# Optimization experiments

Measured on AMD Instinct MI355X. Metric: run time of the kernel, lower is better.

Reference implementation:

```python
import jax, jax.numpy as jnp
import numpy as np

VOXEL_SIZE = (0.2, 0.2, 0.2)
PC_RANGE = (-51.2, -51.2, -3.0, 51.2, 51.2, 3.0)


def setup_inputs() -> dict:
    key = jax.random.key(0)
    # scale so a realistic fraction of points fall outside the z-range / xy-range
    points = jax.random.normal(key, (8, 1_000_000, 3), dtype=jnp.float32) * 20.0
    return {"points": points}


def reference(points):
    # points: [B, N, 3] (x, y, z)
    vs = jnp.asarray(VOXEL_SIZE, dtype=points.dtype)            # [3]
    pcr = jnp.asarray(PC_RANGE, dtype=points.dtype)             # [6]
    min_pt = pcr[:3]
    grid = jnp.round((pcr[3:] - pcr[:3]) / vs).astype(jnp.int32)  # [3] = (512,512,30)

    B, N, _ = points.shape

    # NaN filter (torch: drop rows with any NaN; here: mask them out)
    not_nan = ~jnp.isnan(points).any(axis=-1)                   # [B, N]
    p = jnp.where(not_nan[..., None], points, 0.0)              # NaN-safe points

    # dynamic voxelization: per-point integer voxel coord in (x, y, z) order
    coords_xyz = jnp.floor((p - min_pt) / vs).astype(jnp.int32)  # [B, N, 3]
    in_range = jnp.all((coords_xyz >= 0) & (coords_xyz < grid), axis=-1)  # [B, N]

    valid = not_nan & in_range                                   # [B, N]

    # voxelizer output convention is (z, y, x); invalid points get -1 (as in mmcv)
    coords_zyx = jnp.where(valid[..., None], coords_xyz[..., ::-1], -1)  # [B, N, 3] int32

    # point offsets from voxel centers (computed in x,y,z order, matching
    # torch's voxel_coords[:, [2,1,0]] un-permute)
    centers = coords_xyz.astype(points.dtype) * vs + min_pt + vs / 2
    point_offsets = jnp.where(valid[..., None], p - centers, 0.0)  # [B, N, 3]

    out_points = jnp.where(valid[..., None], p, 0.0)               # [B, N, 3]
    point_idxes = jnp.where(valid, jnp.arange(N, dtype=jnp.int32)[None, :], -1)  # [B, N]

    # masked (fixed-shape) analogue of the per-batch compacted dicts:
    # (points, voxel_coords, point_idxes, point_offsets, valid_mask)
    return out_points, coords_zyx, point_idxes, point_offsets, valid
```

## Files before the change

kernel.cpp:

```cpp
#include <hip/hip_runtime.h>
#include <stdint.h>


#define NPB   1000000
#define TOT   8000000
#define BLK   256
#define PPT   2
#define PPB   (BLK * PPT)
#define NBLK  (TOT / PPB)
#define F4PR  (PPB * 3 / 4)

typedef float fx4 __attribute__((ext_vector_type(4)));

__global__ __launch_bounds__(256, 8) void voxelize_kernel(
        const float* __restrict__ pts, float* __restrict__ out) {
    __shared__ __attribute__((aligned(16))) float lsA[PPB * 3];
    __shared__ __attribute__((aligned(16))) float lsB[PPB * 3];
    __shared__ __attribute__((aligned(16))) float lsC[PPB * 3];

    const int t = threadIdx.x;
    const uint32_t P0 = (uint32_t)blockIdx.x * PPB;

    const double R = 1.0 / (double)0.2f;

    const uint32_t n0  = P0 + (uint32_t)t;
    const uint32_t b0  = n0 / NPB;
    const uint32_t ni0 = n0 - b0 * NPB;

#pragma unroll
    for (int j = 0; j < PPT; ++j) {
        int      pb = j * BLK + t;
        uint32_t n  = P0 + pb;
        uint32_t ni = ni0 + (uint32_t)(j * BLK);
        if (ni >= NPB) ni -= NPB;

        const float* pp = pts + (size_t)n * 3;
        float x = pp[0], y = pp[1], z = pp[2];

        bool nn = (x == x) && (y == y) && (z == z);
        float px = nn ? x : 0.0f;
        float py = nn ? y : 0.0f;
        float pz = nn ? z : 0.0f;

        float tx = (float)((double)(px + 51.2f) * R);
        float ty = (float)((double)(py + 51.2f) * R);
        float tz = (float)((double)(pz + 3.0f)  * R);

        bool valid = nn && (tx >= 0.0f) && (tx < 512.0f)
                        && (ty >= 0.0f) && (ty < 512.0f)
                        && (tz >= 0.0f) && (tz < 30.0f);

        float fcx = truncf(tx);
        float fcy = truncf(ty);
        float fcz = truncf(tz);

        float ctx = (fcx * 0.2f + (-51.2f)) + 0.1f;
        float cty = (fcy * 0.2f + (-51.2f)) + 0.1f;
        float ctz = (fcz * 0.2f + (-3.0f))  + 0.1f;

        lsA[3*pb+0] = valid ? px : 0.0f;
        lsA[3*pb+1] = valid ? py : 0.0f;
        lsA[3*pb+2] = valid ? pz : 0.0f;
        lsB[3*pb+0] = valid ? fcz : -1.0f;
        lsB[3*pb+1] = valid ? fcy : -1.0f;
        lsB[3*pb+2] = valid ? fcx : -1.0f;
        lsC[3*pb+0] = valid ? (px - ctx) : 0.0f;
        lsC[3*pb+1] = valid ? (py - cty) : 0.0f;
        lsC[3*pb+2] = valid ? (pz - ctz) : 0.0f;

        out[(size_t)48000000 + n] = valid ? (float)ni : -1.0f;
        out[(size_t)80000000 + n] = valid ? 1.0f : 0.0f;
    }

    __syncthreads();

    size_t f40 = (size_t)blockIdx.x * F4PR;
#pragma unroll
    for (int i = 0; i < 2; ++i) {
        int li = i * BLK + t;
        if (li < F4PR) {
            size_t f4i = f40 + li;
            fx4 a = ((const fx4*)lsA)[li];
            fx4 c = ((const fx4*)lsB)[li];
            fx4 o = ((const fx4*)lsC)[li];
            ((fx4*)(out))[f4i]                    = a;
            ((fx4*)(out + (size_t)24000000))[f4i] = c;
            ((fx4*)(out + (size_t)56000000))[f4i] = o;
        }
    }
}

extern "C" void kernel_launch(void* const* d_in, const int* in_sizes, int n_in,
                              void* d_out, int out_size, void* d_ws, size_t ws_size,
                              hipStream_t stream) {
    const float* pts = (const float*)d_in[0];
    float* out = (float*)d_out;
    voxelize_kernel<<<NBLK, BLK, 0, stream>>>(pts, out);
}
```

Before: 406.4 us.

## Replace block-wide LDS transpose with per-wavefront staging and wave barriers

Each wavefront now stages its own 64 points' outputs in a private LDS slice and writes them out as float4 vectors right after computing them. This replaces the block-wide __syncthreads and second store loop with wave-level barriers. It also cuts LDS use per block, which may allow more resident blocks, and overlaps stores with computation across iterations. The risk is that wave_barrier ordering of LDS traffic within a wavefront is relied on, and only 48 of 64 lanes store in the vector phase.

```diff
diff --git a/kernel.cpp b/kernel.cpp
--- a/kernel.cpp
+++ b/kernel.cpp
@@ -8,17 +8,19 @@
 #define PPT   2
 #define PPB   (BLK * PPT)
 #define NBLK  (TOT / PPB)
-#define F4PR  (PPB * 3 / 4)
+#define NW    (BLK / 64)
 
 typedef float fx4 __attribute__((ext_vector_type(4)));
 
 __global__ __launch_bounds__(256, 8) void voxelize_kernel(
         const float* __restrict__ pts, float* __restrict__ out) {
-    __shared__ __attribute__((aligned(16))) float lsA[PPB * 3];
-    __shared__ __attribute__((aligned(16))) float lsB[PPB * 3];
-    __shared__ __attribute__((aligned(16))) float lsC[PPB * 3];
+    __shared__ __attribute__((aligned(16))) float lsA[NW * 192];
+    __shared__ __attribute__((aligned(16))) float lsB[NW * 192];
+    __shared__ __attribute__((aligned(16))) float lsC[NW * 192];
 
     const int t = threadIdx.x;
+    const int w = t >> 6;
+    const int l = t & 63;
     const uint32_t P0 = (uint32_t)blockIdx.x * PPB;
 
     const double R = 1.0 / (double)0.2f;
@@ -27,10 +29,13 @@
     const uint32_t b0  = n0 / NPB;
     const uint32_t ni0 = n0 - b0 * NPB;
 
+    float* lA = lsA + w * 192;
+    float* lB = lsB + w * 192;
+    float* lC = lsC + w * 192;
+
 #pragma unroll
     for (int j = 0; j < PPT; ++j) {
-        int      pb = j * BLK + t;
-        uint32_t n  = P0 + pb;
+        uint32_t n  = P0 + (uint32_t)(j * BLK) + (uint32_t)t;
         uint32_t ni = ni0 + (uint32_t)(j * BLK);
         if (ni >= NPB) ni -= NPB;
 
@@ -58,35 +63,33 @@
         float cty = (fcy * 0.2f + (-51.2f)) + 0.1f;
         float ctz = (fcz * 0.2f + (-3.0f))  + 0.1f;
 
-        lsA[3*pb+0] = valid ? px : 0.0f;
-        lsA[3*pb+1] = valid ? py : 0.0f;
-        lsA[3*pb+2] = valid ? pz : 0.0f;
-        lsB[3*pb+0] = valid ? fcz : -1.0f;
-        lsB[3*pb+1] = valid ? fcy : -1.0f;
-        lsB[3*pb+2] = valid ? fcx : -1.0f;
-        lsC[3*pb+0] = valid ? (px - ctx) : 0.0f;
-        lsC[3*pb+1] = valid ? (py - cty) : 0.0f;
-        lsC[3*pb+2] = valid ? (pz - ctz) : 0.0f;
+        lA[3*l+0] = valid ? px : 0.0f;
+        lA[3*l+1] = valid ? py : 0.0f;
+        lA[3*l+2] = valid ? pz : 0.0f;
+        lB[3*l+0] = valid ? fcz : -1.0f;
+        lB[3*l+1] = valid ? fcy : -1.0f;
+        lB[3*l+2] = valid ? fcx : -1.0f;
+        lC[3*l+0] = valid ? (px - ctx) : 0.0f;
+        lC[3*l+1] = valid ? (py - cty) : 0.0f;
+        lC[3*l+2] = valid ? (pz - ctz) : 0.0f;
 
-        out[(size_t)48000000 + n] = valid ? (float)ni : -1.0f;
-        out[(size_t)80000000 + n] = valid ? 1.0f : 0.0f;
-    }
+        __builtin_amdgcn_wave_barrier();
 
-    __syncthreads();
-
-    size_t f40 = (size_t)blockIdx.x * F4PR;
-#pragma unroll
-    for (int i = 0; i < 2; ++i) {
-        int li = i * BLK + t;
-        if (li < F4PR) {
-            size_t f4i = f40 + li;
-            fx4 a = ((const fx4*)lsA)[li];
-            fx4 c = ((const fx4*)lsB)[li];
-            fx4 o = ((const fx4*)lsC)[li];
+        if (l < 48) {
+            fx4 a = ((const fx4*)lA)[l];
+            fx4 c = ((const fx4*)lB)[l];
+            fx4 o = ((const fx4*)lC)[l];
+            size_t f4i = (size_t)blockIdx.x * (PPB * 3 / 4)
+                       + (size_t)(j * 192 + w * 48 + l);
             ((fx4*)(out))[f4i]                    = a;
             ((fx4*)(out + (size_t)24000000))[f4i] = c;
             ((fx4*)(out + (size_t)56000000))[f4i] = o;
         }
+
+        out[(size_t)48000000 + n] = valid ? (float)ni : -1.0f;
+        out[(size_t)80000000 + n] = valid ? 1.0f : 0.0f;
+
+        __builtin_amdgcn_wave_barrier();
     }
 }
 
```

New measurement: 407.3 us. About the same (+0.2%).
